# Performance work log

Measured on AMD Instinct MI355X. Metric: run time of the kernel, lower is better.

## Reference

```python
import jax, jax.numpy as jnp
import numpy as np

B, L, D, K = 4, 8192, 1024, 7
BOUNDARY_PROB = 0.05  # sparse segment boundaries, realistic for token merging


def setup_inputs() -> dict:
    key = jax.random.key(0)
    k1, k2, k3, k4 = jax.random.split(key, 4)
    x = jax.random.normal(k1, (B, L, D), dtype=jnp.float32)
    segment_boundaries = (jax.random.uniform(k2, (B, L)) < BOUNDARY_PROB).astype(jnp.float32)
    # Conv1d(D, D, K, groups=D): weight (out_ch, in_ch/groups, K) = (D, 1, K)
    fan_in = 1 * K
    bound = 1.0 / np.sqrt(fan_in)
    conv_w = jax.random.uniform(k3, (D, 1, K), minval=-bound, maxval=bound, dtype=jnp.float32)
    conv_b = jax.random.uniform(k4, (D,), minval=-bound, maxval=bound, dtype=jnp.float32)
    return {"x": x, "segment_boundaries": segment_boundaries, "conv_w": conv_w, "conv_b": conv_b}


def reference(x, segment_boundaries, conv_w, conv_b):
    # x: (B, L, D); conv_w: (D, 1, K) depthwise; conv_b: (D,)
    b, l, d = x.shape
    k = conv_w.shape[-1]
    half = k // 2

    # torch pads (k-1) on both sides then slices [:L] -> causal conv with left pad k-1
    xc = jnp.transpose(x, (0, 2, 1))  # (B, D, L)
    y = jax.lax.conv_general_dilated(
        xc, conv_w,
        window_strides=(1,),
        padding=[(k - 1, 0)],
        dimension_numbers=("NCH", "OIH", "NCH"),
        feature_group_count=d,
    )  # (B, D, L)
    y = y + conv_b[None, :, None]
    y = jnp.transpose(y, (0, 2, 1))  # (B, L, D)

    # Segment mask: original loop multiplies mask by 0.5 once per boundary whose
    # window [pos-k//2, pos+k//2] (clipped) covers a position -> mask = 0.5**count,
    # count = box-filter(boundaries, width 2*(k//2)+1), zero-padded at edges.
    ones_k = jnp.ones((1, 1, 2 * half + 1), dtype=x.dtype)
    count = jax.lax.conv_general_dilated(
        segment_boundaries[:, None, :], ones_k,
        window_strides=(1,),
        padding=[(half, half)],
        dimension_numbers=("NCH", "OIH", "NCH"),
    )[:, 0, :]  # (B, L)
    mask = jnp.exp2(-count)  # 0.5 ** count

    return y * mask[..., None]
```

## Files before the change

kernel.cpp:

```cpp
#include <hip/hip_runtime.h>

constexpr int B = 4;
constexpr int L = 8192;
constexpr int D = 1024;
constexpr int K = 7;
constexpr int HALF = K / 2;
constexpr int T = 8;
constexpr int W = T + K - 1;
constexpr int NXCD = 8;

typedef float v4f __attribute__((ext_vector_type(4)));

__global__ __launch_bounds__(256, 4)
void dynconv_kernel(const float* __restrict__ x,
                    const float* __restrict__ sb,
                    const float* __restrict__ w,
                    const float* __restrict__ bias,
                    float* __restrict__ out)
{
    constexpr int nwg = B * (L / T);
    constexpr int cpx = nwg / NXCD;
    const int bid  = blockIdx.x;
    const int tile = (bid % NXCD) * cpx + bid / NXCD;

    const int nt  = L / T;
    const int b   = tile / nt;
    const int l0  = (tile % nt) * T;
    const int tid = threadIdx.x;
    const int d0  = tid * 4;

    const float* xb = x + (size_t)b * L * D + d0;
    v4f X[W];
    #pragma unroll
    for (int j = 0; j < W; ++j) {
        const int l = l0 - (K - 1) + j;
        X[j] = (l >= 0) ? *(const v4f*)(xb + (size_t)l * D)
                        : (v4f)(0.f);
    }

    union { v4f q[7]; float f[28]; } wu;
    {
        const v4f* wp = (const v4f*)(w + (size_t)d0 * K);
        #pragma unroll
        for (int j = 0; j < 7; ++j) wu.q[j] = wp[j];
    }
    const v4f bv = *(const v4f*)(bias + d0);

    const float* sbb = sb + (size_t)b * L;
    float s[T + 2 * HALF];
    #pragma unroll
    for (int j = 0; j < T + 2 * HALF; ++j) {
        const int p = l0 - HALF + j;
        s[j] = (p >= 0 && p < L) ? sbb[p] : 0.f;
    }
    float mask[T];
    {
        float c = 0.f;
        #pragma unroll
        for (int j = 0; j < K; ++j) c += s[j];
        mask[0] = exp2f(-c);
        #pragma unroll
        for (int t = 1; t < T; ++t) {
            c += s[t + K - 1] - s[t - 1];
            mask[t] = exp2f(-c);
        }
    }

    float* ob = out + ((size_t)b * L + (size_t)l0) * D + d0;
    #pragma unroll
    for (int t = 0; t < T; ++t) {
        v4f acc = bv;
        #pragma unroll
        for (int k = 0; k < K; ++k) {
            v4f wk = { wu.f[0 * K + k], wu.f[1 * K + k],
                       wu.f[2 * K + k], wu.f[3 * K + k] };
            acc += wk * X[t + k];
        }
        acc *= mask[t];
        __builtin_nontemporal_store(acc, (v4f*)(ob + (size_t)t * D));
    }
}

extern "C" void kernel_launch(void* const* d_in, const int* in_sizes, int n_in,
                              void* d_out, int out_size, void* d_ws, size_t ws_size,
                              hipStream_t stream)
{
    const float* x    = (const float*)d_in[0];
    const float* sb   = (const float*)d_in[1];
    const float* w    = (const float*)d_in[2];
    const float* bias = (const float*)d_in[3];
    float* out = (float*)d_out;

    const int blocks = B * (L / T);
    dynconv_kernel<<<blocks, 256, 0, stream>>>(x, sb, w, bias, out);
}
```

Before: 43.84 us.

## Process four time tiles per block with a sliding register window and prefetch

Each workgroup now covers 32 time steps instead of 8, streaming through four 8-row sub-tiles. The 6-row halo is carried over in registers rather than reloaded, and the next sub-tile's rows are loaded before the current one is computed so memory latency overlaps compute. Halo re-reads drop from 14 rows per 8 outputs to amortized over 32, and per-block weight/bias loads are reduced. The cost is higher register pressure (launch bounds lowered to 3 waves) and a quarter of the blocks, which reduces parallelism.

```diff
diff --git a/kernel.cpp b/kernel.cpp
--- a/kernel.cpp
+++ b/kernel.cpp
@@ -6,37 +6,30 @@
 constexpr int K = 7;
 constexpr int HALF = K / 2;
 constexpr int T = 8;
-constexpr int W = T + K - 1;
+constexpr int P = 4;
+constexpr int SPAN = T * P;
+constexpr int WROW = T + K - 1;
 constexpr int NXCD = 8;
 
 typedef float v4f __attribute__((ext_vector_type(4)));
 
-__global__ __launch_bounds__(256, 4)
+__global__ __launch_bounds__(256, 3)
 void dynconv_kernel(const float* __restrict__ x,
                     const float* __restrict__ sb,
                     const float* __restrict__ w,
                     const float* __restrict__ bias,
                     float* __restrict__ out)
 {
-    constexpr int nwg = B * (L / T);
+    constexpr int nwg = B * (L / SPAN);
     constexpr int cpx = nwg / NXCD;
-    const int bid  = blockIdx.x;
-    const int tile = (bid % NXCD) * cpx + bid / NXCD;
+    const int bid = blockIdx.x;
+    const int st  = (bid % NXCD) * cpx + bid / NXCD;
 
-    const int nt  = L / T;
-    const int b   = tile / nt;
-    const int l0  = (tile % nt) * T;
+    const int spb = L / SPAN;
+    const int b   = st / spb;
+    const int l0  = (st % spb) * SPAN;
     const int tid = threadIdx.x;
     const int d0  = tid * 4;
-
-    const float* xb = x + (size_t)b * L * D + d0;
-    v4f X[W];
-    #pragma unroll
-    for (int j = 0; j < W; ++j) {
-        const int l = l0 - (K - 1) + j;
-        X[j] = (l >= 0) ? *(const v4f*)(xb + (size_t)l * D)
-                        : (v4f)(0.f);
-    }
 
     union { v4f q[7]; float f[28]; } wu;
     {
@@ -46,38 +39,67 @@
     }
     const v4f bv = *(const v4f*)(bias + d0);
 
+    const float* xb  = x  + (size_t)b * L * D + d0;
     const float* sbb = sb + (size_t)b * L;
-    float s[T + 2 * HALF];
+    float*       ob  = out + ((size_t)b * L + (size_t)l0) * D + d0;
+
+    v4f Wn[WROW];
     #pragma unroll
-    for (int j = 0; j < T + 2 * HALF; ++j) {
-        const int p = l0 - HALF + j;
-        s[j] = (p >= 0 && p < L) ? sbb[p] : 0.f;
-    }
-    float mask[T];
-    {
-        float c = 0.f;
-        #pragma unroll
-        for (int j = 0; j < K; ++j) c += s[j];
-        mask[0] = exp2f(-c);
-        #pragma unroll
-        for (int t = 1; t < T; ++t) {
-            c += s[t + K - 1] - s[t - 1];
-            mask[t] = exp2f(-c);
-        }
+    for (int j = 0; j < WROW; ++j) {
+        const int l = l0 - (K - 1) + j;
+        Wn[j] = (l >= 0) ? *(const v4f*)(xb + (size_t)l * D)
+                         : (v4f)(0.f);
     }
 
-    float* ob = out + ((size_t)b * L + (size_t)l0) * D + d0;
     #pragma unroll
-    for (int t = 0; t < T; ++t) {
-        v4f acc = bv;
+    for (int p = 0; p < P; ++p) {
+        const int lp = l0 + p * T;
+
+        v4f N[T];
+        if (p < P - 1) {
+            #pragma unroll
+            for (int i = 0; i < T; ++i)
+                N[i] = *(const v4f*)(xb + (size_t)(lp + T + i) * D);
+        }
+
+        float s[T + 2 * HALF];
         #pragma unroll
-        for (int k = 0; k < K; ++k) {
-            v4f wk = { wu.f[0 * K + k], wu.f[1 * K + k],
-                       wu.f[2 * K + k], wu.f[3 * K + k] };
-            acc += wk * X[t + k];
+        for (int j = 0; j < T + 2 * HALF; ++j) {
+            const int q = lp - HALF + j;
+            s[j] = (q >= 0 && q < L) ? sbb[q] : 0.f;
         }
-        acc *= mask[t];
-        __builtin_nontemporal_store(acc, (v4f*)(ob + (size_t)t * D));
+        float mask[T];
+        {
+            float c = 0.f;
+            #pragma unroll
+            for (int j = 0; j < K; ++j) c += s[j];
+            mask[0] = exp2f(-c);
+            #pragma unroll
+            for (int t = 1; t < T; ++t) {
+                c += s[t + K - 1] - s[t - 1];
+                mask[t] = exp2f(-c);
+            }
+        }
+
+        #pragma unroll
+        for (int t = 0; t < T; ++t) {
+            v4f acc = bv;
+            #pragma unroll
+            for (int k = 0; k < K; ++k) {
+                v4f wk = { wu.f[0 * K + k], wu.f[1 * K + k],
+                           wu.f[2 * K + k], wu.f[3 * K + k] };
+                acc += wk * Wn[t + k];
+            }
+            acc *= mask[t];
+            __builtin_nontemporal_store(acc, (v4f*)(ob + (size_t)(p * T + t) * D));
+        }
+
+        if (p < P - 1) {
+            #pragma unroll
+            for (int j = 0; j < WROW - T; ++j) Wn[j] = Wn[j + T];
+            #pragma unroll
+            for (int i = 0; i < T; ++i)       Wn[WROW - T + i] = N[i];
+        }
     }
 }
 
@@ -91,6 +113,6 @@
     const float* bias = (const float*)d_in[3];
     float* out = (float*)d_out;
 
-    const int blocks = B * (L / T);
+    const int blocks = B * (L / SPAN);
     dynconv_kernel<<<blocks, 256, 0, stream>>>(x, sb, w, bias, out);
 }
```

Measured after the change: 46.98 us. +7.1%, slower.
